# Performance work log

Hardware: AMD Instinct MI355X
Metric: run time of the kernel (lower is better)

Reference implementation:

```python
import jax, jax.numpy as jnp
import numpy as np

N_HEAD, D_MODEL, D_K, D_V, POS_DIM = 8, 512, 64, 64, 2
TEMPERATURE = 8.0
LN_EPS = 1e-6


def setup_inputs() -> dict:
    key = jax.random.key(0)
    ks = jax.random.split(key, 16)
    B, S = 4, 1024
    s = 0.02
    return {
        "q": jax.random.normal(ks[0], (B, S, D_MODEL), jnp.float32),
        "k": jax.random.normal(ks[1], (B, S, D_MODEL), jnp.float32),
        "v": jax.random.normal(ks[2], (B, S, D_MODEL), jnp.float32),
        "pos_mat": jax.random.normal(ks[3], (S, S, POS_DIM), jnp.float32),
        "w_qs": jax.random.normal(ks[4], (N_HEAD * D_K, D_MODEL), jnp.float32) * s,
        "w_ks": jax.random.normal(ks[5], (N_HEAD * D_K, D_MODEL), jnp.float32) * s,
        "w_vs": jax.random.normal(ks[6], (N_HEAD * D_V, D_MODEL), jnp.float32) * s,
        "w_fc": jax.random.normal(ks[7], (D_MODEL, N_HEAD * D_V), jnp.float32) * s,
        "rp_w1": jax.random.normal(ks[8], (D_K, POS_DIM), jnp.float32) * s,
        "rp_b1": jnp.zeros((D_K,), jnp.float32),
        "rp_w2": jax.random.normal(ks[9], (D_K, D_K), jnp.float32) * s,
        "rp_b2": jnp.zeros((D_K,), jnp.float32),
        "ln_g": jnp.ones((D_MODEL,), jnp.float32),
        "ln_b": jnp.zeros((D_MODEL,), jnp.float32),
    }


def reference(q, k, v, pos_mat, w_qs, w_ks, w_vs, w_fc, rp_w1, rp_b1, rp_w2, rp_b2, ln_g, ln_b):
    B, S, _ = q.shape
    residual = q
    # projections -> (b, h, s, d)
    Q = (q @ w_qs.T).reshape(B, S, N_HEAD, D_K).transpose(0, 2, 1, 3)
    K = (k @ w_ks.T).reshape(B, S, N_HEAD, D_K).transpose(0, 2, 1, 3)
    V = (v @ w_vs.T).reshape(B, S, N_HEAD, D_V).transpose(0, 2, 1, 3)
    # relative position embedding: (s, s, d_k)
    a_k = jnp.tanh  # placeholder name avoided; compute MLP (no nonlinearity in original)
    a_k = (pos_mat @ rp_w1.T + rp_b1) @ rp_w2.T + rp_b2
    # sum over d_k of elementwise q*k*a_k, without materializing (b,h,q,k,d)
    attn = jnp.einsum("bhqd,bhkd,qkd->bhqk", Q, K, a_k) / TEMPERATURE
    attn = jax.nn.softmax(attn, axis=-1)  # dropout disabled (eval)
    out = jnp.einsum("bhqk,bhkd->bhqd", attn, V)  # (b,h,s,d_v)
    out = out.transpose(0, 2, 1, 3).reshape(B, S, N_HEAD * D_V)
    out = out @ w_fc.T + residual
    # layer norm
    mu = out.mean(-1, keepdims=True)
    var = out.var(-1, keepdims=True)
    out = (out - mu) / jnp.sqrt(var + LN_EPS) * ln_g + ln_b
    return (out, attn)
```

## Files before the change

### kernel.cpp

```cpp
#include <hip/hip_runtime.h>
#include <math.h>

#define NB   4
#define SEQ  1024
#define DMOD 512
#define NHD  8
#define DK   64

typedef unsigned short ushort_t;
typedef __attribute__((ext_vector_type(8))) short bf16x8;
typedef __attribute__((ext_vector_type(4))) float f32x4;

#define XQ_OFF   1024
#define XK_OFF   (XQ_OFF + 4194304)
#define XV_OFF   (XK_OFF + 4194304)
#define WQ_OFF   (XV_OFF + 4194304)
#define WK_OFF   (WQ_OFF + 524288)
#define WV_OFF   (WK_OFF + 524288)
#define WF_OFF   (WV_OFF + 524288)
#define QBF_OFF  (WF_OFF + 524288)
#define KBF_OFF  (QBF_OFF + 4194304)
#define VT_OFF   (KBF_OFF + 12582912)
#define POSBF_OFF XQ_OFF
#define O2_OFF   XQ_OFF
#define OBF_OFF  XV_OFF


__device__ inline ushort_t f2bf(float x) {
    unsigned u = __builtin_bit_cast(unsigned, x);
    unsigned r = (u + 0x7FFFu + ((u >> 16) & 1u)) >> 16;
    return (ushort_t)r;
}
__device__ inline unsigned pk2(float a, float b) {
    return (unsigned)f2bf(a) | ((unsigned)f2bf(b) << 16);
}

__global__ __launch_bounds__(256)
void setup_kernel(const float* __restrict__ pos,
                  const float* __restrict__ w_qs, const float* __restrict__ w_ks,
                  const float* __restrict__ w_vs, const float* __restrict__ w_fc,
                  const float* __restrict__ rp_w1, const float* __restrict__ rp_b1,
                  const float* __restrict__ rp_w2, const float* __restrict__ rp_b2,
                  unsigned* __restrict__ posbf,
                  ushort_t* __restrict__ WQ, ushort_t* __restrict__ WK,
                  ushort_t* __restrict__ WV, ushort_t* __restrict__ WF,
                  float* __restrict__ ws)
{
    const int bid = blockIdx.x;
    const int tid = threadIdx.x;
    if (bid < 1024) {
        int t = bid * 256 + tid;
        float4 a = *(const float4*)&pos[t * 8];
        float4 b = *(const float4*)&pos[t * 8 + 4];
        uint4 o = {pk2(a.x, a.y), pk2(a.z, a.w), pk2(b.x, b.y), pk2(b.z, b.w)};
        *(uint4*)&posbf[t * 4] = o;
    } else if (bid < 2048) {
        int which = (bid - 1024) >> 8;
        int t = ((bid - 1024) & 255) * 256 + tid;
        const float* s = (which == 0) ? w_qs : (which == 1) ? w_ks
                       : (which == 2) ? w_vs : w_fc;
        ushort_t* d = (which == 0) ? WQ : (which == 1) ? WK
                    : (which == 2) ? WV : WF;
        float4 v = *(const float4*)&s[t * 4];
        uint2 o = {pk2(v.x, v.y), pk2(v.z, v.w)};
        *(uint2*)&d[t * 4] = o;
    } else {
        __shared__ float red[4][64][3];
        int d = tid & 63, p = tid >> 6;
        float w0 = 0.f, w1 = 0.f, cc = 0.f;
        #pragma unroll
        for (int jj = 0; jj < 16; jj++) {
            int j = p * 16 + jj;
            float r2 = rp_w2[d * 64 + j];
            w0 += r2 * rp_w1[j * 2 + 0];
            w1 += r2 * rp_w1[j * 2 + 1];
            cc += r2 * rp_b1[j];
        }
        red[p][d][0] = w0; red[p][d][1] = w1; red[p][d][2] = cc;
        __syncthreads();
        if (p == 0) {
            w0 = red[0][d][0] + red[1][d][0] + red[2][d][0] + red[3][d][0];
            w1 = red[0][d][1] + red[1][d][1] + red[2][d][1] + red[3][d][1];
            cc = red[0][d][2] + red[1][d][2] + red[2][d][2] + red[3][d][2];
            ws[d] = cc + rp_b2[d];
            ws[64 + 2 * d + 0] = w0;
            ws[64 + 2 * d + 1] = w1;
        }
    }
}

#define GP 72

__global__ __launch_bounds__(256)
void mfma_gemm_qkv(const float* __restrict__ xq, const float* __restrict__ xk,
                   const float* __restrict__ xv,
                   const ushort_t* __restrict__ wq, const ushort_t* __restrict__ wk,
                   const ushort_t* __restrict__ wv,
                   ushort_t* __restrict__ Qbf, ushort_t* __restrict__ Kbf,
                   ushort_t* __restrict__ Vt, const float* __restrict__ wc)
{
    __shared__ ushort_t SH[18432];
    const int bz = blockIdx.z;
    const float* X = (bz == 0) ? xq : (bz == 1) ? xk : xv;
    const ushort_t* Wt = (bz == 0) ? wq : (bz == 1) ? wk : wv;
    const int n0 = blockIdx.x * 64;
    const int o0 = blockIdx.y * 64;
    const int tid = threadIdx.x;
    const int wave = tid >> 6, lane = tid & 63;
    const int m16 = lane & 15, g = lane >> 4;
    const int sr = tid >> 3, sc8 = (tid & 7) * 8;

    float4 xa0, xb0, xa1, xb1;
    uint4  wr0, wr1;

#define LOADT(m0_) { \
    xa0 = *(const float4*)&X[(n0 + sr) * 512 + (m0_) + sc8]; \
    xb0 = *(const float4*)&X[(n0 + sr) * 512 + (m0_) + sc8 + 4]; \
    xa1 = *(const float4*)&X[(n0 + sr + 32) * 512 + (m0_) + sc8]; \
    xb1 = *(const float4*)&X[(n0 + sr + 32) * 512 + (m0_) + sc8 + 4]; \
    wr0 = *(const uint4*)&Wt[(o0 + sr) * 512 + (m0_) + sc8]; \
    wr1 = *(const uint4*)&Wt[(o0 + sr + 32) * 512 + (m0_) + sc8]; }
#define STORET(b_) { \
    ushort_t* Xs_ = SH + (b_) * 4608; \
    ushort_t* Ws_ = SH + 9216 + (b_) * 4608; \
    uint4 ox0 = {pk2(xa0.x, xa0.y), pk2(xa0.z, xa0.w), pk2(xb0.x, xb0.y), pk2(xb0.z, xb0.w)}; \
    uint4 ox1 = {pk2(xa1.x, xa1.y), pk2(xa1.z, xa1.w), pk2(xb1.x, xb1.y), pk2(xb1.z, xb1.w)}; \
    *(uint4*)&Xs_[sr * GP + sc8] = ox0; \
    *(uint4*)&Xs_[(sr + 32) * GP + sc8] = ox1; \
    *(uint4*)&Ws_[sr * GP + sc8] = wr0; \
    *(uint4*)&Ws_[(sr + 32) * GP + sc8] = wr1; }

    f32x4 acc[4] = {};
    LOADT(0); STORET(0);
    __syncthreads();
    int cur = 0;
    for (int m0 = 0; m0 < 512; m0 += 64) {
        const int nxt = m0 + 64;
        if (nxt < 512) LOADT(nxt);
        const ushort_t* Xs = SH + cur * 4608;
        const ushort_t* Ws = SH + 9216 + cur * 4608;
        #pragma unroll
        for (int kc = 0; kc < 2; kc++) {
            bf16x8 a = *(const bf16x8*)&Xs[(wave * 16 + m16) * GP + kc * 32 + g * 8];
            #pragma unroll
            for (int to = 0; to < 4; to++) {
                bf16x8 b = *(const bf16x8*)&Ws[(to * 16 + m16) * GP + kc * 32 + g * 8];
                acc[to] = __builtin_amdgcn_mfma_f32_16x16x32_bf16(a, b, acc[to], 0, 0, 0);
            }
        }
        if (nxt < 512) STORET(cur ^ 1);
        __syncthreads();
        cur ^= 1;
    }
#undef LOADT
#undef STORET

    const int b = n0 >> 10, s0 = n0 & 1023, h = o0 >> 6;
    const int bh = b * NHD + h;
    const int srow = wave * 16 + g * 4;

    if (bz == 0) {
        #pragma unroll
        for (int to = 0; to < 4; to++)
            #pragma unroll
            for (int r = 0; r < 4; r++)
                SH[(srow + r) * GP + to * 16 + m16] = f2bf(acc[to][r]);
        __syncthreads();
        #pragma unroll
        for (int it = 0; it < 2; it++) {
            int cid = tid + it * 256;
            int row = cid >> 3, c8 = (cid & 7) * 8;
            *(uint4*)&Qbf[((bh << 10) + s0 + row) * 64 + c8] =
                *(const uint4*)&SH[row * GP + c8];
        }
    } else if (bz == 1) {
        #pragma unroll
        for (int to = 0; to < 4; to++) {
            int d = to * 16 + m16;
            float c0 = wc[d], c1 = wc[64 + 2 * d], c2 = wc[64 + 2 * d + 1];
            #pragma unroll
            for (int r = 0; r < 4; r++) {
                float a = acc[to][r];
                int rb = (srow + r) * 200 + d;
                SH[rb]       = f2bf(a * c0);
                SH[rb + 64]  = f2bf(a * c1);
                SH[rb + 128] = f2bf(a * c2);
            }
        }
        __syncthreads();
        #pragma unroll
        for (int it = 0; it < 6; it++) {
            int cid = tid + it * 256;
            int row = cid / 24, c = cid % 24;
            *(uint4*)&Kbf[((bh << 10) + s0 + row) * 192 + c * 8] =
                *(const uint4*)&SH[row * 200 + c * 8];
        }
    } else {
        #pragma unroll
        for (int to = 0; to < 4; to++)
            #pragma unroll
            for (int r = 0; r < 4; r++)
                SH[(to * 16 + m16) * GP + srow + r] = f2bf(acc[to][r]);
        __syncthreads();
        #pragma unroll
        for (int it = 0; it < 2; it++) {
            int cid = tid + it * 256;
            int row = cid >> 3, c8 = (cid & 7) * 8;
            *(uint4*)&Vt[(bh * 64 + row) * 1024 + s0 + c8] =
                *(const uint4*)&SH[row * GP + c8];
        }
    }
}

__global__ __launch_bounds__(256)
void mfma_gemm_fc(const ushort_t* __restrict__ X, const ushort_t* __restrict__ Wt,
                  float* __restrict__ ofp, const float* __restrict__ resid)
{
    __shared__ ushort_t SH[18432];
    const int n0 = blockIdx.x * 64;
    const int o0 = blockIdx.y * 64;
    const int tid = threadIdx.x;
    const int wave = tid >> 6, lane = tid & 63;
    const int m16 = lane & 15, g = lane >> 4;
    const int sr = tid >> 3, sc8 = (tid & 7) * 8;

    uint4 xr0, xr1, wr0, wr1;

#define LOADF(m0_) { \
    xr0 = *(const uint4*)&X[(n0 + sr) * 512 + (m0_) + sc8]; \
    xr1 = *(const uint4*)&X[(n0 + sr + 32) * 512 + (m0_) + sc8]; \
    wr0 = *(const uint4*)&Wt[(o0 + sr) * 512 + (m0_) + sc8]; \
    wr1 = *(const uint4*)&Wt[(o0 + sr + 32) * 512 + (m0_) + sc8]; }
#define STOREF(b_) { \
    ushort_t* Xs_ = SH + (b_) * 4608; \
    ushort_t* Ws_ = SH + 9216 + (b_) * 4608; \
    *(uint4*)&Xs_[sr * GP + sc8] = xr0; \
    *(uint4*)&Xs_[(sr + 32) * GP + sc8] = xr1; \
    *(uint4*)&Ws_[sr * GP + sc8] = wr0; \
    *(uint4*)&Ws_[(sr + 32) * GP + sc8] = wr1; }

    f32x4 acc[4] = {};
    LOADF(0); STOREF(0);
    __syncthreads();
    int cur = 0;
    for (int m0 = 0; m0 < 512; m0 += 64) {
        const int nxt = m0 + 64;
        if (nxt < 512) LOADF(nxt);
        const ushort_t* Xs = SH + cur * 4608;
        const ushort_t* Ws = SH + 9216 + cur * 4608;
        #pragma unroll
        for (int kc = 0; kc < 2; kc++) {
            bf16x8 a = *(const bf16x8*)&Xs[(wave * 16 + m16) * GP + kc * 32 + g * 8];
            #pragma unroll
            for (int to = 0; to < 4; to++) {
                bf16x8 b = *(const bf16x8*)&Ws[(to * 16 + m16) * GP + kc * 32 + g * 8];
                acc[to] = __builtin_amdgcn_mfma_f32_16x16x32_bf16(a, b, acc[to], 0, 0, 0);
            }
        }
        if (nxt < 512) STOREF(cur ^ 1);
        __syncthreads();
        cur ^= 1;
    }
#undef LOADF
#undef STOREF

    #pragma unroll
    for (int to = 0; to < 4; to++) {
        int o = o0 + to * 16 + m16;
        #pragma unroll
        for (int r = 0; r < 4; r++) {
            int n = n0 + wave * 16 + g * 4 + r;
            ofp[n * 512 + o] = acc[to][r] + resid[n * 512 + o];
        }
    }
}

#define QPITCH 72
#define KPLANE (64 * QPITCH + 8)
#define POSP 68
__global__ __launch_bounds__(256)
void fused_attn(const ushort_t* __restrict__ Qbf, const ushort_t* __restrict__ Kbf,
                const unsigned* __restrict__ posu, const ushort_t* __restrict__ Vt,
                float* __restrict__ attn, ushort_t* __restrict__ Obf)
{
    __shared__ ushort_t Ks[3 * KPLANE];
    __shared__ ushort_t Vs[64 * QPITCH];
    __shared__ ushort_t Ps[64 * QPITCH];
    __shared__ unsigned PosS[64 * POSP];
    const int bh = blockIdx.x;
    const int q0 = blockIdx.y * 64;
    const int tid = threadIdx.x;
    const int wave = tid >> 6, lane = tid & 63;
    const int m16 = lane & 15, g = lane >> 4;

    const ushort_t* qrow = &Qbf[((bh << 10) + q0 + wave * 16 + m16) * 64];
    bf16x8 qf0 = *(const bf16x8*)&qrow[g * 8];
    bf16x8 qf1 = *(const bf16x8*)&qrow[32 + g * 8];

    float l[4] = {0.f, 0.f, 0.f, 0.f};

    for (int k0 = 0; k0 < 1024; k0 += 64) {
        #pragma unroll
        for (int it = 0; it < 6; it++) {
            int idx = tid + it * 256;
            int row = idx / 24, c = idx % 24;
            int j = c >> 3, d8 = (c & 7) * 8;
            *(uint4*)&Ks[j * KPLANE + row * QPITCH + d8] =
                *(const uint4*)&Kbf[((bh << 10) + k0 + row) * 192 + c * 8];
        }
        #pragma unroll
        for (int it = 0; it < 4; it++) {
            int idx = tid + it * 256;
            int row = idx >> 4, c4 = (idx & 15) * 4;
            *(uint4*)&PosS[row * POSP + c4] =
                *(const uint4*)&posu[(q0 + row) * 1024 + k0 + c4];
        }
        __syncthreads();

        f32x4 sc[4][3] = {};
        #pragma unroll
        for (int kc = 0; kc < 2; kc++) {
            bf16x8 af = kc ? qf1 : qf0;
            #pragma unroll
            for (int tk = 0; tk < 4; tk++)
                #pragma unroll
                for (int j = 0; j < 3; j++) {
                    bf16x8 bfv = *(const bf16x8*)&Ks[j * KPLANE + (tk * 16 + m16) * QPITCH + kc * 32 + g * 8];
                    sc[tk][j] = __builtin_amdgcn_mfma_f32_16x16x32_bf16(af, bfv, sc[tk][j], 0, 0, 0);
                }
        }

        #pragma unroll
        for (int r = 0; r < 4; r++) {
            #pragma unroll
            for (int tk = 0; tk < 4; tk++) {
                unsigned pu = PosS[(wave * 16 + g * 4 + r) * POSP + tk * 16 + m16];
                float p0 = __builtin_bit_cast(float, pu << 16);
                float p1 = __builtin_bit_cast(float, pu & 0xFFFF0000u);
                float s = (sc[tk][0][r] + p0 * sc[tk][1][r] + p1 * sc[tk][2][r]) * 0.125f;
                l[r] += __expf(s);
            }
        }
        __syncthreads();
    }
    float inv_l[4];
    #pragma unroll
    for (int r = 0; r < 4; r++) {
        float s = l[r];
        #pragma unroll
        for (int msk = 1; msk < 16; msk <<= 1) s += __shfl_xor(s, msk, 64);
        inv_l[r] = 1.0f / s;
    }

    f32x4 ao[4] = {};
    for (int k0 = 0; k0 < 1024; k0 += 64) {
        #pragma unroll
        for (int it = 0; it < 6; it++) {
            int idx = tid + it * 256;
            int row = idx / 24, c = idx % 24;
            int j = c >> 3, d8 = (c & 7) * 8;
            *(uint4*)&Ks[j * KPLANE + row * QPITCH + d8] =
                *(const uint4*)&Kbf[((bh << 10) + k0 + row) * 192 + c * 8];
        }
        #pragma unroll
        for (int it = 0; it < 2; it++) {
            int idx = tid + it * 256;
            int row = idx >> 3, c8 = (idx & 7) * 8;
            *(uint4*)&Vs[row * QPITCH + c8] = *(const uint4*)&Vt[(bh * 64 + row) * 1024 + k0 + c8];
        }
        #pragma unroll
        for (int it = 0; it < 4; it++) {
            int idx = tid + it * 256;
            int row = idx >> 4, c4 = (idx & 15) * 4;
            *(uint4*)&PosS[row * POSP + c4] =
                *(const uint4*)&posu[(q0 + row) * 1024 + k0 + c4];
        }
        __syncthreads();

        f32x4 sc[4][3] = {};
        #pragma unroll
        for (int kc = 0; kc < 2; kc++) {
            bf16x8 af = kc ? qf1 : qf0;
            #pragma unroll
            for (int tk = 0; tk < 4; tk++)
                #pragma unroll
                for (int j = 0; j < 3; j++) {
                    bf16x8 bfv = *(const bf16x8*)&Ks[j * KPLANE + (tk * 16 + m16) * QPITCH + kc * 32 + g * 8];
                    sc[tk][j] = __builtin_amdgcn_mfma_f32_16x16x32_bf16(af, bfv, sc[tk][j], 0, 0, 0);
                }
        }

        #pragma unroll
        for (int r = 0; r < 4; r++) {
            int q = q0 + wave * 16 + g * 4 + r;
            #pragma unroll
            for (int tk = 0; tk < 4; tk++) {
                unsigned pu = PosS[(wave * 16 + g * 4 + r) * POSP + tk * 16 + m16];
                float p0 = __builtin_bit_cast(float, pu << 16);
                float p1 = __builtin_bit_cast(float, pu & 0xFFFF0000u);
                float s = (sc[tk][0][r] + p0 * sc[tk][1][r] + p1 * sc[tk][2][r]) * 0.125f;
                float p = __expf(s) * inv_l[r];
                attn[((bh << 10) + q) * 1024 + k0 + tk * 16 + m16] = p;
                Ps[(wave * 16 + g * 4 + r) * QPITCH + tk * 16 + m16] = f2bf(p);
            }
        }
        __syncthreads();

        #pragma unroll
        for (int kc = 0; kc < 2; kc++) {
            bf16x8 a = *(const bf16x8*)&Ps[(wave * 16 + m16) * QPITCH + kc * 32 + g * 8];
            #pragma unroll
            for (int td = 0; td < 4; td++) {
                bf16x8 b = *(const bf16x8*)&Vs[(td * 16 + m16) * QPITCH + kc * 32 + g * 8];
                ao[td] = __builtin_amdgcn_mfma_f32_16x16x32_bf16(a, b, ao[td], 0, 0, 0);
            }
        }
        __syncthreads();
    }

    const int b = bh >> 3, h = bh & 7;
    #pragma unroll
    for (int td = 0; td < 4; td++) {
        int d = td * 16 + m16;
        #pragma unroll
        for (int r = 0; r < 4; r++) {
            int q = q0 + wave * 16 + g * 4 + r;
            Obf[((b << 10) + q) * 512 + h * 64 + d] = f2bf(ao[td][r]);
        }
    }
}

__global__ __launch_bounds__(256)
void ln_kernel(const float* __restrict__ X, const float* __restrict__ g,
               const float* __restrict__ bta, float* __restrict__ out)
{
    const int wave = threadIdx.x >> 6, lane = threadIdx.x & 63;
    const int row = blockIdx.x * 4 + wave;
    const int base = row * 512 + lane * 8;
    float4 x0 = *(const float4*)&X[base];
    float4 x1 = *(const float4*)&X[base + 4];
    float s  = x0.x + x0.y + x0.z + x0.w + x1.x + x1.y + x1.z + x1.w;
    float s2 = x0.x * x0.x + x0.y * x0.y + x0.z * x0.z + x0.w * x0.w
             + x1.x * x1.x + x1.y * x1.y + x1.z * x1.z + x1.w * x1.w;
    #pragma unroll
    for (int m = 1; m < 64; m <<= 1) {
        s  += __shfl_xor(s, m, 64);
        s2 += __shfl_xor(s2, m, 64);
    }
    float mu = s * (1.0f / 512.0f);
    float rstd = rsqrtf(s2 * (1.0f / 512.0f) - mu * mu + 1e-6f);
    float4 g0 = *(const float4*)&g[lane * 8];
    float4 g1 = *(const float4*)&g[lane * 8 + 4];
    float4 b0 = *(const float4*)&bta[lane * 8];
    float4 b1 = *(const float4*)&bta[lane * 8 + 4];
    float4 o0, o1;
    o0.x = (x0.x - mu) * rstd * g0.x + b0.x;
    o0.y = (x0.y - mu) * rstd * g0.y + b0.y;
    o0.z = (x0.z - mu) * rstd * g0.z + b0.z;
    o0.w = (x0.w - mu) * rstd * g0.w + b0.w;
    o1.x = (x1.x - mu) * rstd * g1.x + b1.x;
    o1.y = (x1.y - mu) * rstd * g1.y + b1.y;
    o1.z = (x1.z - mu) * rstd * g1.z + b1.z;
    o1.w = (x1.w - mu) * rstd * g1.w + b1.w;
    *(float4*)&out[base] = o0;
    *(float4*)&out[base + 4] = o1;
}

extern "C" void kernel_launch(void* const* d_in, const int* in_sizes, int n_in,
                              void* d_out, int out_size, void* d_ws, size_t ws_size,
                              hipStream_t stream)
{
    const float* q       = (const float*)d_in[0];
    const float* k       = (const float*)d_in[1];
    const float* v       = (const float*)d_in[2];
    const float* pos_mat = (const float*)d_in[3];
    const float* w_qs    = (const float*)d_in[4];
    const float* w_ks    = (const float*)d_in[5];
    const float* w_vs    = (const float*)d_in[6];
    const float* w_fc    = (const float*)d_in[7];
    const float* rp_w1   = (const float*)d_in[8];
    const float* rp_b1   = (const float*)d_in[9];
    const float* rp_w2   = (const float*)d_in[10];
    const float* rp_b2   = (const float*)d_in[11];
    const float* ln_g    = (const float*)d_in[12];
    const float* ln_b    = (const float*)d_in[13];

    char* wsb = (char*)d_ws;
    float*    wc  = (float*)d_ws;
    ushort_t* WQ  = (ushort_t*)(wsb + WQ_OFF);
    ushort_t* WK  = (ushort_t*)(wsb + WK_OFF);
    ushort_t* WV  = (ushort_t*)(wsb + WV_OFF);
    ushort_t* WF  = (ushort_t*)(wsb + WF_OFF);
    ushort_t* Qbf = (ushort_t*)(wsb + QBF_OFF);
    ushort_t* Kbf = (ushort_t*)(wsb + KBF_OFF);
    ushort_t* Vt  = (ushort_t*)(wsb + VT_OFF);
    float*    O2  = (float*)(wsb + O2_OFF);
    ushort_t* Obf = (ushort_t*)(wsb + OBF_OFF);
    unsigned* Pbf = (unsigned*)(wsb + POSBF_OFF);

    float* out  = (float*)d_out;
    float* attn = out + 2097152;

    setup_kernel<<<dim3(2049), 256, 0, stream>>>(pos_mat, w_qs, w_ks, w_vs, w_fc,
                                                 rp_w1, rp_b1, rp_w2, rp_b2,
                                                 Pbf, WQ, WK, WV, WF, wc);

    mfma_gemm_qkv<<<dim3(64, 8, 3), 256, 0, stream>>>(q, k, v, WQ, WK, WV,
                                                      Qbf, Kbf, Vt, wc);

    fused_attn<<<dim3(32, 16), 256, 0, stream>>>(Qbf, Kbf, Pbf, Vt, attn, Obf);

    mfma_gemm_fc<<<dim3(64, 8), 256, 0, stream>>>(Obf, WF, O2, q);
    ln_kernel<<<dim3(1024), 256, 0, stream>>>(O2, ln_g, ln_b, out);
}
```

Baseline: 282.0 us.

## Halve attention query tile to 32 and split key columns across waves

Each attention block now handles 32 query rows instead of 64, which doubles the grid to 1024 blocks. Within a block, each wave now owns a 16-column key slice for both 16-row query halves, where before it owned a 16-row query slice across all keys. Row sums are combined across waves through a small shared-memory reduction, and each wave computes a 16-wide slice of the output dimension. This aims to raise occupancy and parallelism on the GPU, at the cost of loading K, V and the K-projection planes twice as often per query row, which doubles L2/HBM traffic for K.

```diff
diff --git a/kernel.cpp b/kernel.cpp
--- a/kernel.cpp
+++ b/kernel.cpp
@@ -285,19 +285,24 @@
 {
     __shared__ ushort_t Ks[3 * KPLANE];
     __shared__ ushort_t Vs[64 * QPITCH];
-    __shared__ ushort_t Ps[64 * QPITCH];
-    __shared__ unsigned PosS[64 * POSP];
+    __shared__ ushort_t Ps[32 * QPITCH];
+    __shared__ unsigned PosS[32 * POSP];
+    __shared__ float Lred[4][2][4][4];
     const int bh = blockIdx.x;
-    const int q0 = blockIdx.y * 64;
+    const int q0 = blockIdx.y * 32;
     const int tid = threadIdx.x;
     const int wave = tid >> 6, lane = tid & 63;
     const int m16 = lane & 15, g = lane >> 4;
 
-    const ushort_t* qrow = &Qbf[((bh << 10) + q0 + wave * 16 + m16) * 64];
-    bf16x8 qf0 = *(const bf16x8*)&qrow[g * 8];
-    bf16x8 qf1 = *(const bf16x8*)&qrow[32 + g * 8];
-
-    float l[4] = {0.f, 0.f, 0.f, 0.f};
+    bf16x8 qf[2][2];
+    #pragma unroll
+    for (int qh = 0; qh < 2; qh++) {
+        const ushort_t* qrow = &Qbf[((bh << 10) + q0 + qh * 16 + m16) * 64];
+        qf[qh][0] = *(const bf16x8*)&qrow[g * 8];
+        qf[qh][1] = *(const bf16x8*)&qrow[32 + g * 8];
+    }
+
+    float l[2][4] = {};
 
     for (int k0 = 0; k0 < 1024; k0 += 64) {
         #pragma unroll
@@ -309,7 +314,7 @@
                 *(const uint4*)&Kbf[((bh << 10) + k0 + row) * 192 + c * 8];
         }
         #pragma unroll
-        for (int it = 0; it < 4; it++) {
+        for (int it = 0; it < 2; it++) {
             int idx = tid + it * 256;
             int row = idx >> 4, c4 = (idx & 15) * 4;
             *(uint4*)&PosS[row * POSP + c4] =
@@ -317,42 +322,51 @@
         }
         __syncthreads();
 
-        f32x4 sc[4][3] = {};
+        f32x4 sc[2][3] = {};
         #pragma unroll
         for (int kc = 0; kc < 2; kc++) {
-            bf16x8 af = kc ? qf1 : qf0;
-            #pragma unroll
-            for (int tk = 0; tk < 4; tk++)
+            #pragma unroll
+            for (int qh = 0; qh < 2; qh++) {
+                bf16x8 af = qf[qh][kc];
                 #pragma unroll
                 for (int j = 0; j < 3; j++) {
-                    bf16x8 bfv = *(const bf16x8*)&Ks[j * KPLANE + (tk * 16 + m16) * QPITCH + kc * 32 + g * 8];
-                    sc[tk][j] = __builtin_amdgcn_mfma_f32_16x16x32_bf16(af, bfv, sc[tk][j], 0, 0, 0);
+                    bf16x8 bfv = *(const bf16x8*)&Ks[j * KPLANE + (wave * 16 + m16) * QPITCH + kc * 32 + g * 8];
+                    sc[qh][j] = __builtin_amdgcn_mfma_f32_16x16x32_bf16(af, bfv, sc[qh][j], 0, 0, 0);
                 }
-        }
-
-        #pragma unroll
-        for (int r = 0; r < 4; r++) {
-            #pragma unroll
-            for (int tk = 0; tk < 4; tk++) {
-                unsigned pu = PosS[(wave * 16 + g * 4 + r) * POSP + tk * 16 + m16];
+            }
+        }
+
+        #pragma unroll
+        for (int qh = 0; qh < 2; qh++)
+            #pragma unroll
+            for (int r = 0; r < 4; r++) {
+                unsigned pu = PosS[(qh * 16 + g * 4 + r) * POSP + wave * 16 + m16];
                 float p0 = __builtin_bit_cast(float, pu << 16);
                 float p1 = __builtin_bit_cast(float, pu & 0xFFFF0000u);
-                float s = (sc[tk][0][r] + p0 * sc[tk][1][r] + p1 * sc[tk][2][r]) * 0.125f;
-                l[r] += __expf(s);
-            }
-        }
-        __syncthreads();
-    }
-    float inv_l[4];
+                float s = (sc[qh][0][r] + p0 * sc[qh][1][r] + p1 * sc[qh][2][r]) * 0.125f;
+                l[qh][r] += __expf(s);
+            }
+        __syncthreads();
+    }
     #pragma unroll
-    for (int r = 0; r < 4; r++) {
-        float s = l[r];
-        #pragma unroll
-        for (int msk = 1; msk < 16; msk <<= 1) s += __shfl_xor(s, msk, 64);
-        inv_l[r] = 1.0f / s;
-    }
-
-    f32x4 ao[4] = {};
+    for (int qh = 0; qh < 2; qh++)
+        #pragma unroll
+        for (int r = 0; r < 4; r++) {
+            float s = l[qh][r];
+            #pragma unroll
+            for (int msk = 1; msk < 16; msk <<= 1) s += __shfl_xor(s, msk, 64);
+            if (m16 == 0) Lred[wave][qh][g][r] = s;
+        }
+    __syncthreads();
+    float inv_l[2][4];
+    #pragma unroll
+    for (int qh = 0; qh < 2; qh++)
+        #pragma unroll
+        for (int r = 0; r < 4; r++)
+            inv_l[qh][r] = 1.0f / (Lred[0][qh][g][r] + Lred[1][qh][g][r] +
+                                   Lred[2][qh][g][r] + Lred[3][qh][g][r]);
+
+    f32x4 ao[2] = {};
     for (int k0 = 0; k0 < 1024; k0 += 64) {
         #pragma unroll
         for (int it = 0; it < 6; it++) {
@@ -369,7 +383,7 @@
             *(uint4*)&Vs[row * QPITCH + c8] = *(const uint4*)&Vt[(bh * 64 + row) * 1024 + k0 + c8];
         }
         #pragma unroll
-        for (int it = 0; it < 4; it++) {
+        for (int it = 0; it < 2; it++) {
             int idx = tid + it * 256;
             int row = idx >> 4, c4 = (idx & 15) * 4;
             *(uint4*)&PosS[row * POSP + c4] =
@@ -377,42 +391,42 @@
         }
         __syncthreads();
 
-        f32x4 sc[4][3] = {};
+        f32x4 sc[2][3] = {};
         #pragma unroll
         for (int kc = 0; kc < 2; kc++) {
-            bf16x8 af = kc ? qf1 : qf0;
-            #pragma unroll
-            for (int tk = 0; tk < 4; tk++)
+            #pragma unroll
+            for (int qh = 0; qh < 2; qh++) {
+                bf16x8 af = qf[qh][kc];
                 #pragma unroll
                 for (int j = 0; j < 3; j++) {
-                    bf16x8 bfv = *(const bf16x8*)&Ks[j * KPLANE + (tk * 16 + m16) * QPITCH + kc * 32 + g * 8];
-                    sc[tk][j] = __builtin_amdgcn_mfma_f32_16x16x32_bf16(af, bfv, sc[tk][j], 0, 0, 0);
+                    bf16x8 bfv = *(const bf16x8*)&Ks[j * KPLANE + (wave * 16 + m16) * QPITCH + kc * 32 + g * 8];
+                    sc[qh][j] = __builtin_amdgcn_mfma_f32_16x16x32_bf16(af, bfv, sc[qh][j], 0, 0, 0);
                 }
-        }
-
-        #pragma unroll
-        for (int r = 0; r < 4; r++) {
-            int q = q0 + wave * 16 + g * 4 + r;
-            #pragma unroll
-            for (int tk = 0; tk < 4; tk++) {
-                unsigned pu = PosS[(wave * 16 + g * 4 + r) * POSP + tk * 16 + m16];
+            }
+        }
+
+        #pragma unroll
+        for (int qh = 0; qh < 2; qh++)
+            #pragma unroll
+            for (int r = 0; r < 4; r++) {
+                int q = q0 + qh * 16 + g * 4 + r;
+                unsigned pu = PosS[(qh * 16 + g * 4 + r) * POSP + wave * 16 + m16];
                 float p0 = __builtin_bit_cast(float, pu << 16);
                 float p1 = __builtin_bit_cast(float, pu & 0xFFFF0000u);
-                float s = (sc[tk][0][r] + p0 * sc[tk][1][r] + p1 * sc[tk][2][r]) * 0.125f;
-                float p = __expf(s) * inv_l[r];
-                attn[((bh << 10) + q) * 1024 + k0 + tk * 16 + m16] = p;
-                Ps[(wave * 16 + g * 4 + r) * QPITCH + tk * 16 + m16] = f2bf(p);
-            }
-        }
+                float s = (sc[qh][0][r] + p0 * sc[qh][1][r] + p1 * sc[qh][2][r]) * 0.125f;
+                float p = __expf(s) * inv_l[qh][r];
+                attn[((bh << 10) + q) * 1024 + k0 + wave * 16 + m16] = p;
+                Ps[(qh * 16 + g * 4 + r) * QPITCH + wave * 16 + m16] = f2bf(p);
+            }
         __syncthreads();
 
         #pragma unroll
         for (int kc = 0; kc < 2; kc++) {
-            bf16x8 a = *(const bf16x8*)&Ps[(wave * 16 + m16) * QPITCH + kc * 32 + g * 8];
-            #pragma unroll
-            for (int td = 0; td < 4; td++) {
-                bf16x8 b = *(const bf16x8*)&Vs[(td * 16 + m16) * QPITCH + kc * 32 + g * 8];
-                ao[td] = __builtin_amdgcn_mfma_f32_16x16x32_bf16(a, b, ao[td], 0, 0, 0);
+            #pragma unroll
+            for (int qh = 0; qh < 2; qh++) {
+                bf16x8 a = *(const bf16x8*)&Ps[(qh * 16 + m16) * QPITCH + kc * 32 + g * 8];
+                bf16x8 b = *(const bf16x8*)&Vs[(wave * 16 + m16) * QPITCH + kc * 32 + g * 8];
+                ao[qh] = __builtin_amdgcn_mfma_f32_16x16x32_bf16(a, b, ao[qh], 0, 0, 0);
             }
         }
         __syncthreads();
@@ -420,14 +434,12 @@
 
     const int b = bh >> 3, h = bh & 7;
     #pragma unroll
-    for (int td = 0; td < 4; td++) {
-        int d = td * 16 + m16;
+    for (int qh = 0; qh < 2; qh++)
         #pragma unroll
         for (int r = 0; r < 4; r++) {
-            int q = q0 + wave * 16 + g * 4 + r;
-            Obf[((b << 10) + q) * 512 + h * 64 + d] = f2bf(ao[td][r]);
-        }
-    }
+            int q = q0 + qh * 16 + g * 4 + r;
+            Obf[((b << 10) + q) * 512 + h * 64 + wave * 16 + m16] = f2bf(ao[qh][r]);
+        }
 }
 
 __global__ __launch_bounds__(256)
@@ -508,7 +520,7 @@
     mfma_gemm_qkv<<<dim3(64, 8, 3), 256, 0, stream>>>(q, k, v, WQ, WK, WV,
                                                       Qbf, Kbf, Vt, wc);
 
-    fused_attn<<<dim3(32, 16), 256, 0, stream>>>(Qbf, Kbf, Pbf, Vt, attn, Obf);
+    fused_attn<<<dim3(32, 32), 256, 0, stream>>>(Qbf, Kbf, Pbf, Vt, attn, Obf);
 
     mfma_gemm_fc<<<dim3(64, 8), 256, 0, stream>>>(Obf, WF, O2, q);
     ln_kernel<<<dim3(1024), 256, 0, stream>>>(O2, ln_g, ln_b, out);
```

Result: slower. 298.8 us (+6.0%).
